# Performance work log

Measured on AMD Instinct MI355X. Metric: run time of the kernel, lower is better.

The kernel has to match this reference:

```python
import jax, jax.numpy as jnp
import numpy as np

N = 50000      # nodes
E = 800000     # edges (avg degree 16)
F_IN = 128
HID = 64
NCLS = 40
K = 2          # num_stacks
T = 2          # num_layers (shared weights)


def setup_inputs() -> dict:
    key = jax.random.key(0)
    ks = jax.random.split(key, 10)
    s = 0.05
    return {
        "x": jax.random.normal(ks[0], (N, F_IN), dtype=jnp.float32),
        "edge_index": jax.random.randint(ks[1], (2, E), 0, N),
        "w1_init": jax.random.normal(ks[2], (K, F_IN, HID), dtype=jnp.float32) * s,
        "w1": jax.random.normal(ks[3], (K, HID, HID), dtype=jnp.float32) * s,
        "v1": jax.random.normal(ks[4], (K, F_IN, HID), dtype=jnp.float32) * s,
        "b1": jax.random.normal(ks[5], (K, HID), dtype=jnp.float32) * s,
        "w2_init": jax.random.normal(ks[6], (K, HID, NCLS), dtype=jnp.float32) * s,
        "w2": jax.random.normal(ks[7], (K, NCLS, NCLS), dtype=jnp.float32) * s,
        "v2": jax.random.normal(ks[8], (K, HID, NCLS), dtype=jnp.float32) * s,
        "b2": jax.random.normal(ks[9], (K, NCLS), dtype=jnp.float32) * s,
    }


def _gcn_norm(src, dst, n):
    # PyG gcn_norm with add_self_loops=False: deg over destination, sym norm
    deg = jax.ops.segment_sum(jnp.ones_like(dst, dtype=jnp.float32), dst, num_segments=n)
    dinv = jnp.where(deg > 0, 1.0 / jnp.sqrt(deg), 0.0)
    return dinv[src] * dinv[dst]  # [E]


def _arma_conv(x, src, dst, norm, n, w_init, w, v, b, act):
    # x: [N, Fin]; w_init: [K, Fin, Fout]; w: [K, Fout, Fout]; v: [K, Fin, Fout]; b: [K, Fout]
    root = jnp.einsum('nf,kfg->kng', x, v)  # [K, N, Fout], dropout=0 -> identity
    out = None
    for t in range(T):
        if t == 0:
            h = jnp.einsum('nf,kfg->kng', x, w_init)
        else:
            h = jnp.einsum('knf,kfg->kng', out, w)
        # sparse neighbor aggregation: out[i] = sum_{(j->i)} norm_e * h[j]
        agg = jax.vmap(
            lambda hk: jax.ops.segment_sum(hk[src] * norm[:, None], dst, num_segments=n)
        )(h)  # [K, N, Fout]
        out = act(agg + root + b[:, None, :])
    return out.mean(axis=0)  # mean over stacks -> [N, Fout]


def reference(x, edge_index, w1_init, w1, v1, b1, w2_init, w2, v2, b2):
    src, dst = edge_index[0], edge_index[1]
    norm = _gcn_norm(src, dst, N)
    h = _arma_conv(x, src, dst, norm, N, w1_init, w1, v1, b1, jax.nn.relu)
    h = jax.nn.relu(h)  # wrapper ReLU; dropout is identity in eval
    o = _arma_conv(h, src, dst, norm, N, w2_init, w2, v2, b2, lambda z: z)
    return jax.nn.log_softmax(o, axis=1)
```

## Files before the change

### kernel.cpp

```cpp
#include <hip/hip_runtime.h>
#include <hip/hip_bf16.h>
#include <math.h>

#define N_NODES 50000
#define F_IN 128
#define HID 64
#define NCLS 40
#define K_STACKS 2
#define SCAN_TILE 1024
#define NBLK_CNT 256

typedef __attribute__((ext_vector_type(8))) short short8;
typedef __attribute__((ext_vector_type(4))) float floatx4;
typedef __attribute__((ext_vector_type(2))) float floatx2;

__device__ __forceinline__ unsigned int f32_to_bf16_bits(float f) {
    unsigned int u = __float_as_uint(f);
    return (u + 0x7fffu + ((u >> 16) & 1u)) >> 16;
}
__device__ __forceinline__ unsigned int pack_bf16x2(float a, float b) {
    return f32_to_bf16_bits(a) | (f32_to_bf16_bits(b) << 16);
}
__device__ __forceinline__ unsigned char f32_to_fp8(float v) {
    int pk = __builtin_amdgcn_cvt_pk_fp8_f32(v, v, 0, false);
    return (unsigned char)(pk & 0xff);
}


__global__ __launch_bounds__(256) void count_kernel(const int* __restrict__ dst,
                                                    int* __restrict__ counts,
                                                    int* __restrict__ tileSums, int E) {
    __shared__ int hist[256];
    __shared__ int ts[64];
    int blk = blockIdx.x, t = threadIdx.x;
    hist[t] = 0;
    if (t < 64) ts[t] = 0;
    __syncthreads();
    int chunk = (E + NBLK_CNT - 1) / NBLK_CNT;
    int s = blk * chunk, e = min(E, s + chunk);
    for (int i = s + t; i < e; i += 256) atomicAdd(&hist[dst[i] >> 8], 1);
    __syncthreads();
    counts[t * NBLK_CNT + blk] = hist[t];
    atomicAdd(&ts[t >> 2], hist[t]);
    __syncthreads();
    if (t < 64) atomicAdd(&tileSums[t], ts[t]);
}

__global__ __launch_bounds__(256) void scan_phase3_excl(const int* __restrict__ in,
                                                        const int* __restrict__ tileSums,
                                                        int* __restrict__ out, int n) {
    __shared__ int lds[256];
    __shared__ int tsum[64];
    int b = blockIdx.x, t = threadIdx.x;
    if (t < 64) tsum[t] = tileSums[t];
    int base = b * SCAN_TILE + t * 4;
    int e[4];
    int s = 0;
#pragma unroll
    for (int i = 0; i < 4; ++i) {
        e[i] = (base + i < n) ? in[base + i] : 0;
        s += e[i];
    }
    lds[t] = s;
    __syncthreads();
    int v = s;
    for (int off = 1; off < 256; off <<= 1) {
        int add = (t >= off) ? lds[t - off] : 0;
        __syncthreads();
        v += add;
        lds[t] = v;
        __syncthreads();
    }
    int toff = 0;
    for (int i = 0; i < b; ++i) toff += tsum[i];
    int run = (t == 0 ? 0 : lds[t - 1]) + toff;
#pragma unroll
    for (int i = 0; i < 4; ++i) {
        if (base + i < n) {
            out[base + i] = run;
            run += e[i];
        }
    }
}

__global__ __launch_bounds__(256) void bucket_scatter_kernel(const int* __restrict__ src,
                                                             const int* __restrict__ dst,
                                                             const int* __restrict__ scanned,
                                                             unsigned int* __restrict__ pairs,
                                                             int E) {
    __shared__ int cur[256];
    int blk = blockIdx.x, t = threadIdx.x;
    cur[t] = scanned[t * NBLK_CNT + blk];
    __syncthreads();
    int chunk = (E + NBLK_CNT - 1) / NBLK_CNT;
    int s0 = blk * chunk, e0 = min(E, s0 + chunk);
    for (int i = s0 + t; i < e0; i += 256) {
        int d = dst[i];
        int pos = atomicAdd(&cur[d >> 8], 1);
        pairs[pos] = (unsigned int)src[i] | ((unsigned int)(d & 255) << 16);
    }
}

__global__ __launch_bounds__(256) void csr_build_kernel(const unsigned int* __restrict__ pairs,
                                                        const int* __restrict__ scanned,
                                                        int* __restrict__ row_ptr,
                                                        float* __restrict__ dinv,
                                                        int* __restrict__ col, int N, int E) {
    __shared__ int degl[256], lds[256], curl[256], sb[2];
    int b = blockIdx.x, t = threadIdx.x;
    if (t == 0) {
        sb[0] = scanned[b * NBLK_CNT];
        sb[1] = (b + 1 < 256) ? scanned[(b + 1) * NBLK_CNT] : E;
    }
    degl[t] = 0;
    __syncthreads();
    int bstart = sb[0], bend = sb[1];
    for (int e = bstart + t; e < bend; e += 256) {
        atomicAdd(&degl[(pairs[e] >> 16) & 255], 1);
    }
    __syncthreads();
    int d = degl[t];
    lds[t] = d;
    __syncthreads();
    int v = d;
    for (int off = 1; off < 256; off <<= 1) {
        int add = (t >= off) ? lds[t - off] : 0;
        __syncthreads();
        v += add;
        lds[t] = v;
        __syncthreads();
    }
    int excl = v - d;
    int node = b * 256 + t;
    if (node <= N) row_ptr[node] = bstart + excl;
    if (node < N) dinv[node] = (d > 0) ? (1.0f / sqrtf((float)d)) : 0.0f;
    curl[t] = excl;
    __syncthreads();
    for (int e = bstart + t; e < bend; e += 256) {
        unsigned int p = pairs[e];
        int ln = (p >> 16) & 255;
        int pos = atomicAdd(&curl[ln], 1);
        col[bstart + pos] = (int)(p & 0xffffu);
    }
}

__device__ __forceinline__ void wt_one(const float* __restrict__ in,
                                       unsigned short* __restrict__ out, int li, int C, int F,
                                       int CP) {
    int k = li / (F * CP);
    int r = li - k * F * CP;
    int f = r / CP;
    int c = r - f * CP;
    out[li] = (c < C) ? (unsigned short)f32_to_bf16_bits(in[((size_t)k * C + c) * F + f]) : 0;
}

__global__ void wt_all_kernel(const float* v1, const float* w1i, const float* w1,
                              const float* v2, const float* w2i, const float* w2,
                              unsigned short* v1t, unsigned short* w1it, unsigned short* w1t,
                              unsigned short* v2t, unsigned short* w2it, unsigned short* w2t) {
    int i = blockIdx.x * blockDim.x + threadIdx.x;
    if (i < 16384) wt_one(v1, v1t, i, 128, 64, 128);
    else if (i < 32768) wt_one(w1i, w1it, i - 16384, 128, 64, 128);
    else if (i < 40960) wt_one(w1, w1t, i - 32768, 64, 64, 64);
    else if (i < 46080) wt_one(v2, v2t, i - 40960, 64, 40, 64);
    else if (i < 51200) wt_one(w2i, w2it, i - 46080, 64, 40, 64);
    else if (i < 56320) wt_one(w2, w2t, i - 51200, 40, 40, 64);
}

template <int CINP>
__device__ __forceinline__ void stage_A(const void* A, unsigned short* At, size_t abase,
                                        int n0, int t, int N, int CREAL, int a_bf16,
                                        int stride) {
    constexpr int CP8 = CINP / 8;
    constexpr int MS = CP8 - 1;
    constexpr int SH = (CP8 == 16) ? 4 : 3;
    for (int i = t; i < 64 * CP8; i += stride) {
        int n = i >> SH;
        int c = i & MS;
        uint4 w = make_uint4(0u, 0u, 0u, 0u);
        int gn = n0 + n;
        if (gn < N && c * 8 < CREAL) {
            if (a_bf16) {
                w = *(const uint4*)((const unsigned short*)A + abase + (size_t)gn * CREAL + c * 8);
            } else {
                const float* srcp = (const float*)A + abase + (size_t)gn * CREAL + c * 8;
                float4 f0 = *(const float4*)(srcp);
                float4 f1 = *(const float4*)(srcp + 4);
                w.x = pack_bf16x2(f0.x, f0.y);
                w.y = pack_bf16x2(f0.z, f0.w);
                w.z = pack_bf16x2(f1.x, f1.y);
                w.w = pack_bf16x2(f1.z, f1.w);
            }
        }
        *(uint4*)(At + n * CINP + ((c ^ (n & MS)) << 3)) = w;
    }
}

template <int CINP>
__device__ __forceinline__ void stage_B(const unsigned short* Bk, unsigned short* Bs, int t,
                                        int COUT, int stride) {
    constexpr int CP8 = CINP / 8;
    constexpr int MS = CP8 - 1;
    constexpr int SH = (CP8 == 16) ? 4 : 3;
    for (int i = t; i < COUT * CP8; i += stride) {
        int f = i >> SH;
        int c = i & MS;
        uint4 w = *(const uint4*)(Bk + f * CINP + c * 8);
        *(uint4*)(Bs + f * CINP + ((c ^ (f & MS)) << 3)) = w;
    }
}

__global__ __launch_bounds__(512) void gemm2k(
    const float* __restrict__ A, const unsigned short* __restrict__ Bt1,
    const unsigned short* __restrict__ Bt2, unsigned short* __restrict__ out1,
    unsigned char* __restrict__ out2, const float* __restrict__ scale, int N) {
    constexpr int CINP = 128;
    constexpr int MS = 15;
    __shared__ __align__(16) unsigned short At[64 * CINP];

    const int n0 = blockIdx.x * 64;
    const int t = threadIdx.x;
    stage_A<CINP>(A, At, (size_t)0, n0, t, N, CINP, 0, 512);
    __syncthreads();

    const int lane = t & 63;
    const int wv = t >> 6;
    const int kSel = wv >> 2;
    const int m0 = (wv & 3) * 16;
    const int quad = lane >> 4;
    const int li = lane & 15;
    const int am = (m0 + li) & MS;
    const unsigned short* B1k = Bt1 + (size_t)kSel * 64 * CINP;
    const unsigned short* B2k = Bt2 + (size_t)kSel * 64 * CINP;

    floatx4 acc1[4] = {{0.f, 0.f, 0.f, 0.f}, {0.f, 0.f, 0.f, 0.f},
                       {0.f, 0.f, 0.f, 0.f}, {0.f, 0.f, 0.f, 0.f}};
    floatx4 acc2[4] = {{0.f, 0.f, 0.f, 0.f}, {0.f, 0.f, 0.f, 0.f},
                       {0.f, 0.f, 0.f, 0.f}, {0.f, 0.f, 0.f, 0.f}};
#pragma unroll
    for (int kc = 0; kc < 4; ++kc) {
        int cc = kc * 4 + quad;
        short8 a = *(const short8*)(At + (m0 + li) * CINP + ((cc ^ am) << 3));
#pragma unroll
        for (int nt = 0; nt < 4; ++nt) {
            int f = nt * 16 + li;
            size_t bo = (size_t)f * CINP + cc * 8;
            short8 b1 = *(const short8*)(B1k + bo);
            short8 b2 = *(const short8*)(B2k + bo);
            acc1[nt] = __builtin_amdgcn_mfma_f32_16x16x32_bf16(a, b1, acc1[nt], 0, 0, 0);
            acc2[nt] = __builtin_amdgcn_mfma_f32_16x16x32_bf16(a, b2, acc2[nt], 0, 0, 0);
        }
    }

    float sc[4];
#pragma unroll
    for (int r = 0; r < 4; ++r) {
        int node = n0 + m0 + quad * 4 + r;
        sc[r] = (node < N) ? scale[node] : 1.f;
    }
#pragma unroll
    for (int nt = 0; nt < 4; ++nt) {
        int f = nt * 16 + li;
#pragma unroll
        for (int r = 0; r < 4; ++r) {
            int node = n0 + m0 + quad * 4 + r;
            if (node < N) {
                out1[((size_t)kSel * N + node) * 64 + f] =
                    (unsigned short)f32_to_bf16_bits(acc1[nt][r]);
                out2[(size_t)node * 128 + (size_t)kSel * 64 + f] =
                    f32_to_fp8(acc2[nt][r] * sc[r]);
            }
        }
    }
}

template <int F, int COUT, int FMODE>
__global__ __launch_bounds__(512) void agg_gemm_kernel(
    const unsigned char* __restrict__ h8, const int* __restrict__ row_ptr,
    const int* __restrict__ col, const float* __restrict__ dinv,
    const unsigned short* __restrict__ rootb, const float* __restrict__ bias,
    const unsigned short* __restrict__ Bt1, const unsigned short* __restrict__ Bt2,
    unsigned short* __restrict__ rootOut, unsigned char* __restrict__ tblOut, int N) {
    constexpr int NA = (FMODE == 1) ? 1 : 2;
    constexpr int NB = (FMODE == 1) ? 4 : 2;
    constexpr int BT = COUT * 64;
    constexpr int NT = (COUT + 15) / 16;
    constexpr int FH = F / 8;
    constexpr int ROWB = 2 * F;
    __shared__ __align__(16) unsigned short At[NA * 64 * 64];
    __shared__ __align__(16) unsigned short Bs[NB * BT];
    __shared__ int rp[65];
    __shared__ float dvl[64];

    const int n0 = blockIdx.x * 64;
    const int t = threadIdx.x;

    stage_B<64>(Bt1, Bs, t, COUT, 512);
    stage_B<64>(Bt1 + (size_t)COUT * 64, Bs + BT, t, COUT, 512);
    if constexpr (FMODE == 1) {
        stage_B<64>(Bt2, Bs + 2 * BT, t, COUT, 512);
        stage_B<64>(Bt2 + (size_t)COUT * 64, Bs + 3 * BT, t, COUT, 512);
    }
    if (t < 65) rp[t] = row_ptr[min(n0 + t, N)];
    if (t < 64) dvl[t] = (n0 + t < N) ? dinv[n0 + t] : 0.f;
    __syncthreads();

    const int lane = t & 63;
    const int wv = t >> 6;
    const int half = lane >> 5;
    const int l32 = lane & 31;
    const int sub = l32 >> 4;
    const int fq = l32 & 15;
    const int kk = fq >> 3;
    const int fqq = fq & 7;
    const int fqc = (fqq < FH) ? fqq : (FH - 1);
    const int foff = kk * F + fqc * 8;

#pragma unroll 1
    for (int p = 0; p < 4; ++p) {
        const int nl = wv * 8 + p * 2 + half;
        const int node = n0 + nl;
        const bool valid = node < N;
        const int e0 = rp[nl];
        const int deg = rp[nl + 1] - e0;
        const float dv = dvl[nl];
        float acc[8] = {};
        for (int w0 = 0; w0 < deg; w0 += 32) {
            int mye = w0 + l32;
            int c = (mye < deg) ? col[e0 + mye] : 0;
            int nch = min(deg - w0, 32);
            for (int base = 0; base < nch; base += 16) {
                uint2 v[8];
                float wj[8];
#pragma unroll
                for (int u = 0; u < 8; ++u) {
                    int j = base + u * 2 + sub;
                    int cj = __shfl(c, (half << 5) | (j & 31));
                    bool ok = (j < nch);
                    wj[u] = ok ? 1.f : 0.f;
                    int cs = ok ? cj : 0;
                    v[u] = *(const uint2*)(h8 + (size_t)cs * ROWB + foff);
                }
#pragma unroll
                for (int u = 0; u < 8; ++u) {
                    floatx2 f0 = __builtin_amdgcn_cvt_pk_f32_fp8(v[u].x, false);
                    floatx2 f1 = __builtin_amdgcn_cvt_pk_f32_fp8(v[u].x, true);
                    floatx2 f2 = __builtin_amdgcn_cvt_pk_f32_fp8(v[u].y, false);
                    floatx2 f3 = __builtin_amdgcn_cvt_pk_f32_fp8(v[u].y, true);
                    acc[0] += wj[u] * f0.x;
                    acc[1] += wj[u] * f0.y;
                    acc[2] += wj[u] * f1.x;
                    acc[3] += wj[u] * f1.y;
                    acc[4] += wj[u] * f2.x;
                    acc[5] += wj[u] * f2.y;
                    acc[6] += wj[u] * f3.x;
                    acc[7] += wj[u] * f3.y;
                }
            }
        }
#pragma unroll
        for (int i = 0; i < 8; ++i) acc[i] += __shfl_xor(acc[i], 16);

        size_t oc = ((size_t)kk * N + (valid ? node : 0)) * F + fqc * 8;
        uint4 rv = *(const uint4*)(rootb + oc);
        const float* bp = bias + kk * F + fqc * 8;
        float4 b0 = *(const float4*)(bp);
        float4 b1_ = *(const float4*)(bp + 4);
        const unsigned int ru[4] = {rv.x, rv.y, rv.z, rv.w};
        float res[8];
#pragma unroll
        for (int q = 0; q < 4; ++q) {
            float rlo = __uint_as_float(ru[q] << 16);
            float rhi = __uint_as_float(ru[q] & 0xffff0000u);
            float blo = (q < 2) ? ((q == 0) ? b0.x : b0.z) : ((q == 2) ? b1_.x : b1_.z);
            float bhi = (q < 2) ? ((q == 0) ? b0.y : b0.w) : ((q == 2) ? b1_.y : b1_.w);
            res[2 * q] = acc[2 * q] * dv + rlo + blo;
            res[2 * q + 1] = acc[2 * q + 1] * dv + rhi + bhi;
        }
        if constexpr (FMODE != 2) {
#pragma unroll
            for (int i = 0; i < 8; ++i) res[i] = fmaxf(res[i], 0.f);
        }
        if constexpr (FMODE == 1) {
            float mres[8];
#pragma unroll
            for (int i = 0; i < 8; ++i) mres[i] = 0.5f * (res[i] + __shfl_xor(res[i], 8));
            if (sub == 0 && kk == 0) {
                uint4 w;
                w.x = pack_bf16x2(mres[0], mres[1]);
                w.y = pack_bf16x2(mres[2], mres[3]);
                w.z = pack_bf16x2(mres[4], mres[5]);
                w.w = pack_bf16x2(mres[6], mres[7]);
                *(uint4*)(At + nl * 64 + ((fqq ^ (nl & 7)) << 3)) = w;
            }
        } else {
            if (sub == 0) {
                uint4 w = make_uint4(0u, 0u, 0u, 0u);
                if (fqq < FH) {
                    w.x = pack_bf16x2(res[0], res[1]);
                    w.y = pack_bf16x2(res[2], res[3]);
                    w.z = pack_bf16x2(res[4], res[5]);
                    w.w = pack_bf16x2(res[6], res[7]);
                }
                *(uint4*)(At + kk * 4096 + nl * 64 + ((fqq ^ (nl & 7)) << 3)) = w;
            }
        }
    }
    __syncthreads();

    const int quad = lane >> 4;
    const int li = lane & 15;
    const int kSel = wv >> 2;
    const int m0 = (wv & 3) * 16;
    const int am = (m0 + li) & 7;

    if constexpr (FMODE == 1) {
        floatx4 aR[NT] = {};
        floatx4 aT[NT] = {};
#pragma unroll
        for (int kc = 0; kc < 2; ++kc) {
            int cc = kc * 4 + quad;
            short8 a = *(const short8*)(At + (m0 + li) * 64 + ((cc ^ am) << 3));
#pragma unroll
            for (int nt = 0; nt < NT; ++nt) {
                int f = nt * 16 + li;
                int fc = (COUT & 15) ? ((f < COUT) ? f : (COUT - 1)) : f;
                int bo = fc * 64 + ((cc ^ (fc & 7)) << 3);
                short8 bR = *(const short8*)(Bs + kSel * BT + bo);
                short8 bT = *(const short8*)(Bs + (2 + kSel) * BT + bo);
                aR[nt] = __builtin_amdgcn_mfma_f32_16x16x32_bf16(a, bR, aR[nt], 0, 0, 0);
                aT[nt] = __builtin_amdgcn_mfma_f32_16x16x32_bf16(a, bT, aT[nt], 0, 0, 0);
            }
        }
#pragma unroll
        for (int nt = 0; nt < NT; ++nt) {
            int f = nt * 16 + li;
            if (f >= COUT) continue;
#pragma unroll
            for (int r = 0; r < 4; ++r) {
                int nl2 = m0 + quad * 4 + r;
                int node = n0 + nl2;
                if (node < N) {
                    rootOut[((size_t)kSel * N + node) * COUT + f] =
                        (unsigned short)f32_to_bf16_bits(aR[nt][r]);
                    tblOut[(size_t)node * 2 * COUT + (size_t)kSel * COUT + f] =
                        f32_to_fp8(aT[nt][r] * dvl[nl2]);
                }
            }
        }
    } else {
        floatx4 ac[NT] = {};
#pragma unroll
        for (int kc = 0; kc < 2; ++kc) {
            int cc = kc * 4 + quad;
            short8 a = *(const short8*)(At + kSel * 4096 + (m0 + li) * 64 + ((cc ^ am) << 3));
#pragma unroll
            for (int nt = 0; nt < NT; ++nt) {
                int f = nt * 16 + li;
                int fc = (COUT & 15) ? ((f < COUT) ? f : (COUT - 1)) : f;
                int bo = fc * 64 + ((cc ^ (fc & 7)) << 3);
                short8 b = *(const short8*)(Bs + kSel * BT + bo);
                ac[nt] = __builtin_amdgcn_mfma_f32_16x16x32_bf16(a, b, ac[nt], 0, 0, 0);
            }
        }
#pragma unroll
        for (int nt = 0; nt < NT; ++nt) {
            int f = nt * 16 + li;
            if (f >= COUT) continue;
#pragma unroll
            for (int r = 0; r < 4; ++r) {
                int nl2 = m0 + quad * 4 + r;
                int node = n0 + nl2;
                if (node < N)
                    tblOut[(size_t)node * 2 * COUT + (size_t)kSel * COUT + f] =
                        f32_to_fp8(ac[nt][r] * dvl[nl2]);
            }
        }
    }
}

template <int F>
__global__ __launch_bounds__(256) void agg_kernel(
    const unsigned char* __restrict__ h8, const int* __restrict__ row_ptr,
    const int* __restrict__ col, const float* __restrict__ dinv,
    const unsigned short* __restrict__ rootb, const float* __restrict__ bias,
    void* __restrict__ out, int N, int do_relu, int mode) {
    constexpr int FH = F / 8;
    constexpr int ROWB = 2 * F;
    int wid = (blockIdx.x * blockDim.x + threadIdx.x) >> 6;
    int lane = threadIdx.x & 63;
    int half = lane >> 5;
    int l32 = lane & 31;
    int node = wid * 2 + half;
    bool valid = node < N;
    int e0 = 0, deg = 0;
    float dv = 0.f;
    if (valid) {
        e0 = row_ptr[node];
        deg = row_ptr[node + 1] - e0;
        dv = dinv[node];
    }
    const int sub = l32 >> 4;
    const int fq = l32 & 15;
    const int kk = fq >> 3;
    const int fqq = fq & 7;
    const int fqc = (fqq < FH) ? fqq : (FH - 1);
    const int foff = kk * F + fqc * 8;

    float acc[8] = {};
    for (int w0 = 0; w0 < deg; w0 += 32) {
        int mye = w0 + l32;
        int c = (mye < deg) ? col[e0 + mye] : 0;
        int nch = min(deg - w0, 32);
        for (int base = 0; base < nch; base += 16) {
            uint2 v[8];
            float wj[8];
#pragma unroll
            for (int u = 0; u < 8; ++u) {
                int j = base + u * 2 + sub;
                int cj = __shfl(c, (half << 5) | (j & 31));
                bool ok = (j < nch);
                wj[u] = ok ? 1.f : 0.f;
                int cs = ok ? cj : 0;
                v[u] = *(const uint2*)(h8 + (size_t)cs * ROWB + foff);
            }
#pragma unroll
            for (int u = 0; u < 8; ++u) {
                floatx2 f0 = __builtin_amdgcn_cvt_pk_f32_fp8(v[u].x, false);
                floatx2 f1 = __builtin_amdgcn_cvt_pk_f32_fp8(v[u].x, true);
                floatx2 f2 = __builtin_amdgcn_cvt_pk_f32_fp8(v[u].y, false);
                floatx2 f3 = __builtin_amdgcn_cvt_pk_f32_fp8(v[u].y, true);
                acc[0] += wj[u] * f0.x;
                acc[1] += wj[u] * f0.y;
                acc[2] += wj[u] * f1.x;
                acc[3] += wj[u] * f1.y;
                acc[4] += wj[u] * f2.x;
                acc[5] += wj[u] * f2.y;
                acc[6] += wj[u] * f3.x;
                acc[7] += wj[u] * f3.y;
            }
        }
    }
#pragma unroll
    for (int i = 0; i < 8; ++i) acc[i] += __shfl_xor(acc[i], 16);

    size_t oc = ((size_t)kk * N + (valid ? node : 0)) * F + fqc * 8;
    uint4 rv = *(const uint4*)(rootb + oc);
    const float* bp = bias + kk * F + fqc * 8;
    float4 b0 = *(const float4*)(bp);
    float4 b1 = *(const float4*)(bp + 4);
    const unsigned int ru[4] = {rv.x, rv.y, rv.z, rv.w};
    float res[8];
#pragma unroll
    for (int q = 0; q < 4; ++q) {
        float rlo = __uint_as_float(ru[q] << 16);
        float rhi = __uint_as_float(ru[q] & 0xffff0000u);
        float blo = (q < 2) ? ((q == 0) ? b0.x : b0.z) : ((q == 2) ? b1.x : b1.z);
        float bhi = (q < 2) ? ((q == 0) ? b0.y : b0.w) : ((q == 2) ? b1.y : b1.w);
        res[2 * q] = acc[2 * q] * dv + rlo + blo;
        res[2 * q + 1] = acc[2 * q + 1] * dv + rhi + bhi;
    }
    if (do_relu) {
#pragma unroll
        for (int i = 0; i < 8; ++i) res[i] = fmaxf(res[i], 0.f);
    }
    if (mode == 0) {
        if (sub == 0 && fqq < FH && valid) {
            size_t o = ((size_t)kk * N + node) * F + fqq * 8;
            uint4 w;
            w.x = pack_bf16x2(res[0], res[1]);
            w.y = pack_bf16x2(res[2], res[3]);
            w.z = pack_bf16x2(res[4], res[5]);
            w.w = pack_bf16x2(res[6], res[7]);
            *(uint4*)((unsigned short*)out + o) = w;
        }
    } else {
        float mres[8];
#pragma unroll
        for (int i = 0; i < 8; ++i) mres[i] = 0.5f * (res[i] + __shfl_xor(res[i], 8));
        if (mode == 1) {
            if (sub == 0 && kk == 0 && fqq < FH && valid) {
                size_t o = (size_t)node * F + fqq * 8;
                *(float4*)((float*)out + o) = make_float4(mres[0], mres[1], mres[2], mres[3]);
                *(float4*)((float*)out + o + 4) = make_float4(mres[4], mres[5], mres[6], mres[7]);
            }
        } else {
            bool act = (fqq < FH);
            float lm = -INFINITY;
            if (act) {
#pragma unroll
                for (int i = 0; i < 8; ++i) lm = fmaxf(lm, mres[i]);
            }
#pragma unroll
            for (int m = 1; m < 8; m <<= 1) lm = fmaxf(lm, __shfl_xor(lm, m));
            float ls = 0.f;
            if (act) {
#pragma unroll
                for (int i = 0; i < 8; ++i) ls += expf(mres[i] - lm);
            }
#pragma unroll
            for (int m = 1; m < 8; m <<= 1) ls += __shfl_xor(ls, m);
            float lg = lm + logf(ls);
            if (sub == 0 && kk == 0 && act && valid) {
                size_t o = (size_t)node * F + fqq * 8;
                *(float4*)((float*)out + o) =
                    make_float4(mres[0] - lg, mres[1] - lg, mres[2] - lg, mres[3] - lg);
                *(float4*)((float*)out + o + 4) =
                    make_float4(mres[4] - lg, mres[5] - lg, mres[6] - lg, mres[7] - lg);
            }
        }
    }
}


static inline size_t align256(size_t x) { return (x + 255) & ~(size_t)255; }

extern "C" void kernel_launch(void* const* d_in, const int* in_sizes, int n_in,
                              void* d_out, int out_size, void* d_ws, size_t ws_size,
                              hipStream_t stream) {
    const float* x = (const float*)d_in[0];
    const int* ei = (const int*)d_in[1];
    const float* w1_init = (const float*)d_in[2];
    const float* w1 = (const float*)d_in[3];
    const float* v1 = (const float*)d_in[4];
    const float* b1 = (const float*)d_in[5];
    const float* w2_init = (const float*)d_in[6];
    const float* w2 = (const float*)d_in[7];
    const float* v2 = (const float*)d_in[8];
    const float* b2 = (const float*)d_in[9];

    const int N = in_sizes[0] / F_IN;
    const int E = in_sizes[1] / 2;
    const int* src = ei;
    const int* dst = ei + E;

    char* p = (char*)d_ws;
    auto take = [&](size_t bytes) {
        char* r = p;
        p += align256(bytes);
        return r;
    };
    float* dinv = (float*)take((size_t)N * 4);
    int* row_ptr = (int*)take((size_t)(N + 1) * 4);
    int* tileSums = (int*)take(256 * 4);
    int* counts = (int*)take((size_t)256 * NBLK_CNT * 4);
    int* scanned = (int*)take((size_t)256 * NBLK_CNT * 4);
    unsigned int* pairs = (unsigned int*)take((size_t)E * 4);
    int* col = (int*)take((size_t)E * 4);
    unsigned short* v1t = (unsigned short*)take((size_t)2 * 64 * 128 * 2);
    unsigned short* w1it = (unsigned short*)take((size_t)2 * 64 * 128 * 2);
    unsigned short* w1t = (unsigned short*)take((size_t)2 * 64 * 64 * 2);
    unsigned short* v2t = (unsigned short*)take((size_t)2 * 40 * 64 * 2);
    unsigned short* w2it = (unsigned short*)take((size_t)2 * 40 * 64 * 2);
    unsigned short* w2t = (unsigned short*)take((size_t)2 * 40 * 64 * 2);
    unsigned short* rootb = (unsigned short*)take((size_t)K_STACKS * N * HID * 2);
    unsigned short* root2 = (unsigned short*)take((size_t)K_STACKS * N * NCLS * 2);
    unsigned char* tblA = (unsigned char*)take((size_t)K_STACKS * N * HID);
    unsigned char* tblB = (unsigned char*)take((size_t)K_STACKS * N * HID);

    const int TB = 256;
    const int nCnt = 256 * NBLK_CNT;
    const int nScanBlocks = nCnt / SCAN_TILE;
    const int nBuckets = (N + 255) / 256;
    const int ntiles = (N + 63) / 64;

    hipMemsetAsync(tileSums, 0, 256, stream);
    count_kernel<<<NBLK_CNT, 256, 0, stream>>>(dst, counts, tileSums, E);
    scan_phase3_excl<<<nScanBlocks, 256, 0, stream>>>(counts, tileSums, scanned, nCnt);
    bucket_scatter_kernel<<<NBLK_CNT, 256, 0, stream>>>(src, dst, scanned, pairs, E);
    csr_build_kernel<<<nBuckets, 256, 0, stream>>>(pairs, scanned, row_ptr, dinv, col, N, E);

    wt_all_kernel<<<(56320 + TB - 1) / TB, TB, 0, stream>>>(v1, w1_init, w1, v2, w2_init, w2,
                                                            v1t, w1it, w1t, v2t, w2it, w2t);

    const int agg_blocks = ((N + 1) / 2 + 3) / 4;

    gemm2k<<<ntiles, 512, 0, stream>>>(x, v1t, w1it, rootb, tblA, dinv, N);
    agg_gemm_kernel<HID, HID, 0><<<ntiles, 512, 0, stream>>>(
        tblA, row_ptr, col, dinv, rootb, b1, w1t, nullptr, nullptr, tblB, N);

    agg_gemm_kernel<HID, NCLS, 1><<<ntiles, 512, 0, stream>>>(
        tblB, row_ptr, col, dinv, rootb, b1, v2t, w2it, root2, tblA, N);

    agg_gemm_kernel<NCLS, NCLS, 2><<<ntiles, 512, 0, stream>>>(
        tblA, row_ptr, col, dinv, root2, b2, w2t, nullptr, nullptr, tblB, N);

    agg_kernel<NCLS><<<agg_blocks, 256, 0, stream>>>(tblB, row_ptr, col, dinv, root2, b2,
                                                     (float*)d_out, N, 0, 2);
}
```

Measured before the change: 276.0 us.

## Drop LDS weight staging, process two rows per gather pass, fold memset into weight kernel

The fused aggregate+GEMM kernels no longer copy the B weight matrices into shared memory. MFMA operands are now read straight from global memory (expected to be cache-resident), which cuts LDS use, and the launch bounds request 4 blocks per CU. The neighbour gather now walks two destination rows at once, so more independent loads are in flight, and padding lanes are zeroed by select instead of multiply. The tileSums memset is folded into the weight-transpose kernel, which moves ahead of the CSR build, removing one launch. The risks are uncoalesced global B reads, more register pressure from the doubled accumulators, and wasted work when the two rows differ in degree.

```diff
diff --git a/kernel.cpp b/kernel.cpp
--- a/kernel.cpp
+++ b/kernel.cpp
@@ -157,8 +157,10 @@
 __global__ void wt_all_kernel(const float* v1, const float* w1i, const float* w1,
                               const float* v2, const float* w2i, const float* w2,
                               unsigned short* v1t, unsigned short* w1it, unsigned short* w1t,
-                              unsigned short* v2t, unsigned short* w2it, unsigned short* w2t) {
+                              unsigned short* v2t, unsigned short* w2it, unsigned short* w2t,
+                              int* tileSums) {
     int i = blockIdx.x * blockDim.x + threadIdx.x;
+    if (blockIdx.x == 0 && threadIdx.x < 64) tileSums[threadIdx.x] = 0;
     if (i < 16384) wt_one(v1, v1t, i, 128, 64, 128);
     else if (i < 32768) wt_one(w1i, w1it, i - 16384, 128, 64, 128);
     else if (i < 40960) wt_one(w1, w1t, i - 32768, 64, 64, 64);
@@ -196,20 +198,6 @@
     }
 }
 
-template <int CINP>
-__device__ __forceinline__ void stage_B(const unsigned short* Bk, unsigned short* Bs, int t,
-                                        int COUT, int stride) {
-    constexpr int CP8 = CINP / 8;
-    constexpr int MS = CP8 - 1;
-    constexpr int SH = (CP8 == 16) ? 4 : 3;
-    for (int i = t; i < COUT * CP8; i += stride) {
-        int f = i >> SH;
-        int c = i & MS;
-        uint4 w = *(const uint4*)(Bk + f * CINP + c * 8);
-        *(uint4*)(Bs + f * CINP + ((c ^ (f & MS)) << 3)) = w;
-    }
-}
-
 __global__ __launch_bounds__(512) void gemm2k(
     const float* __restrict__ A, const unsigned short* __restrict__ Bt1,
     const unsigned short* __restrict__ Bt2, unsigned short* __restrict__ out1,
@@ -275,34 +263,28 @@
 }
 
 template <int F, int COUT, int FMODE>
-__global__ __launch_bounds__(512) void agg_gemm_kernel(
+__global__ __launch_bounds__(512, 4) void agg_gemm_kernel(
     const unsigned char* __restrict__ h8, const int* __restrict__ row_ptr,
     const int* __restrict__ col, const float* __restrict__ dinv,
     const unsigned short* __restrict__ rootb, const float* __restrict__ bias,
     const unsigned short* __restrict__ Bt1, const unsigned short* __restrict__ Bt2,
     unsigned short* __restrict__ rootOut, unsigned char* __restrict__ tblOut, int N) {
     constexpr int NA = (FMODE == 1) ? 1 : 2;
-    constexpr int NB = (FMODE == 1) ? 4 : 2;
-    constexpr int BT = COUT * 64;
     constexpr int NT = (COUT + 15) / 16;
     constexpr int FH = F / 8;
     constexpr int ROWB = 2 * F;
     __shared__ __align__(16) unsigned short At[NA * 64 * 64];
-    __shared__ __align__(16) unsigned short Bs[NB * BT];
     __shared__ int rp[65];
     __shared__ float dvl[64];
 
     const int n0 = blockIdx.x * 64;
     const int t = threadIdx.x;
 
-    stage_B<64>(Bt1, Bs, t, COUT, 512);
-    stage_B<64>(Bt1 + (size_t)COUT * 64, Bs + BT, t, COUT, 512);
-    if constexpr (FMODE == 1) {
-        stage_B<64>(Bt2, Bs + 2 * BT, t, COUT, 512);
-        stage_B<64>(Bt2 + (size_t)COUT * 64, Bs + 3 * BT, t, COUT, 512);
-    }
     if (t < 65) rp[t] = row_ptr[min(n0 + t, N)];
-    if (t < 64) dvl[t] = (n0 + t < N) ? dinv[n0 + t] : 0.f;
+    if (t >= 128 && t < 192) {
+        int i = t - 128;
+        dvl[i] = (n0 + i < N) ? dinv[n0 + i] : 0.f;
+    }
     __syncthreads();
 
     const int lane = t & 63;
@@ -316,51 +298,12 @@
     const int fqc = (fqq < FH) ? fqq : (FH - 1);
     const int foff = kk * F + fqc * 8;
 
-#pragma unroll 1
-    for (int p = 0; p < 4; ++p) {
-        const int nl = wv * 8 + p * 2 + half;
+    auto finish_row = [&](int nl, float* acc) {
         const int node = n0 + nl;
         const bool valid = node < N;
-        const int e0 = rp[nl];
-        const int deg = rp[nl + 1] - e0;
         const float dv = dvl[nl];
-        float acc[8] = {};
-        for (int w0 = 0; w0 < deg; w0 += 32) {
-            int mye = w0 + l32;
-            int c = (mye < deg) ? col[e0 + mye] : 0;
-            int nch = min(deg - w0, 32);
-            for (int base = 0; base < nch; base += 16) {
-                uint2 v[8];
-                float wj[8];
-#pragma unroll
-                for (int u = 0; u < 8; ++u) {
-                    int j = base + u * 2 + sub;
-                    int cj = __shfl(c, (half << 5) | (j & 31));
-                    bool ok = (j < nch);
-                    wj[u] = ok ? 1.f : 0.f;
-                    int cs = ok ? cj : 0;
-                    v[u] = *(const uint2*)(h8 + (size_t)cs * ROWB + foff);
-                }
-#pragma unroll
-                for (int u = 0; u < 8; ++u) {
-                    floatx2 f0 = __builtin_amdgcn_cvt_pk_f32_fp8(v[u].x, false);
-                    floatx2 f1 = __builtin_amdgcn_cvt_pk_f32_fp8(v[u].x, true);
-                    floatx2 f2 = __builtin_amdgcn_cvt_pk_f32_fp8(v[u].y, false);
-                    floatx2 f3 = __builtin_amdgcn_cvt_pk_f32_fp8(v[u].y, true);
-                    acc[0] += wj[u] * f0.x;
-                    acc[1] += wj[u] * f0.y;
-                    acc[2] += wj[u] * f1.x;
-                    acc[3] += wj[u] * f1.y;
-                    acc[4] += wj[u] * f2.x;
-                    acc[5] += wj[u] * f2.y;
-                    acc[6] += wj[u] * f3.x;
-                    acc[7] += wj[u] * f3.y;
-                }
-            }
-        }
 #pragma unroll
         for (int i = 0; i < 8; ++i) acc[i] += __shfl_xor(acc[i], 16);
-
         size_t oc = ((size_t)kk * N + (valid ? node : 0)) * F + fqc * 8;
         uint4 rv = *(const uint4*)(rootb + oc);
         const float* bp = bias + kk * F + fqc * 8;
@@ -405,6 +348,68 @@
                 *(uint4*)(At + kk * 4096 + nl * 64 + ((fqq ^ (nl & 7)) << 3)) = w;
             }
         }
+    };
+
+#pragma unroll 1
+    for (int p = 0; p < 2; ++p) {
+        const int nlA = wv * 8 + p * 4 + half;
+        const int nlB = nlA + 2;
+        const int e0A = rp[nlA];
+        const int degA = rp[nlA + 1] - e0A;
+        const int e0B = rp[nlB];
+        const int degB = rp[nlB + 1] - e0B;
+        const int degM = max(degA, degB);
+        float accA[8] = {};
+        float accB[8] = {};
+        for (int w0 = 0; w0 < degM; w0 += 32) {
+            int mye = w0 + l32;
+            int cA = (mye < degA) ? col[e0A + mye] : 0;
+            int cB = (mye < degB) ? col[e0B + mye] : 0;
+            int nchA = degA - w0;
+            int nchB = degB - w0;
+            if (nchA > 32) nchA = 32;
+            if (nchB > 32) nchB = 32;
+            int nchM = min(degM - w0, 32);
+            for (int base = 0; base < nchM; base += 16) {
+                uint2 vA[8], vB[8];
+#pragma unroll
+                for (int u = 0; u < 8; ++u) {
+                    int j = base + u * 2 + sub;
+                    int li32 = (half << 5) | (j & 31);
+                    int cjA = __shfl(cA, li32);
+                    int cjB = __shfl(cB, li32);
+                    bool okA = (j < nchA);
+                    bool okB = (j < nchB);
+                    uint2 tA = *(const uint2*)(h8 + (size_t)(okA ? cjA : 0) * ROWB + foff);
+                    uint2 tB = *(const uint2*)(h8 + (size_t)(okB ? cjB : 0) * ROWB + foff);
+                    vA[u].x = okA ? tA.x : 0u;
+                    vA[u].y = okA ? tA.y : 0u;
+                    vB[u].x = okB ? tB.x : 0u;
+                    vB[u].y = okB ? tB.y : 0u;
+                }
+#pragma unroll
+                for (int u = 0; u < 8; ++u) {
+                    floatx2 a0 = __builtin_amdgcn_cvt_pk_f32_fp8(vA[u].x, false);
+                    floatx2 a1 = __builtin_amdgcn_cvt_pk_f32_fp8(vA[u].x, true);
+                    floatx2 a2 = __builtin_amdgcn_cvt_pk_f32_fp8(vA[u].y, false);
+                    floatx2 a3 = __builtin_amdgcn_cvt_pk_f32_fp8(vA[u].y, true);
+                    accA[0] += a0.x; accA[1] += a0.y;
+                    accA[2] += a1.x; accA[3] += a1.y;
+                    accA[4] += a2.x; accA[5] += a2.y;
+                    accA[6] += a3.x; accA[7] += a3.y;
+                    floatx2 c0 = __builtin_amdgcn_cvt_pk_f32_fp8(vB[u].x, false);
+                    floatx2 c1 = __builtin_amdgcn_cvt_pk_f32_fp8(vB[u].x, true);
+                    floatx2 c2 = __builtin_amdgcn_cvt_pk_f32_fp8(vB[u].y, false);
+                    floatx2 c3 = __builtin_amdgcn_cvt_pk_f32_fp8(vB[u].y, true);
+                    accB[0] += c0.x; accB[1] += c0.y;
+                    accB[2] += c1.x; accB[3] += c1.y;
+                    accB[4] += c2.x; accB[5] += c2.y;
+                    accB[6] += c3.x; accB[7] += c3.y;
+                }
+            }
+        }
+        finish_row(nlA, accA);
+        finish_row(nlB, accB);
     }
     __syncthreads();
 
@@ -413,8 +418,10 @@
     const int kSel = wv >> 2;
     const int m0 = (wv & 3) * 16;
     const int am = (m0 + li) & 7;
+    const unsigned short* B1k = Bt1 + (size_t)kSel * COUT * 64;
 
     if constexpr (FMODE == 1) {
+        const unsigned short* B2k = Bt2 + (size_t)kSel * COUT * 64;
         floatx4 aR[NT] = {};
         floatx4 aT[NT] = {};
 #pragma unroll
@@ -424,10 +431,10 @@
 #pragma unroll
             for (int nt = 0; nt < NT; ++nt) {
                 int f = nt * 16 + li;
-                int fc = (COUT & 15) ? ((f < COUT) ? f : (COUT - 1)) : f;
-                int bo = fc * 64 + ((cc ^ (fc & 7)) << 3);
-                short8 bR = *(const short8*)(Bs + kSel * BT + bo);
-                short8 bT = *(const short8*)(Bs + (2 + kSel) * BT + bo);
+                int fc = (f < COUT) ? f : (COUT - 1);
+                size_t bo = (size_t)fc * 64 + cc * 8;
+                short8 bR = *(const short8*)(B1k + bo);
+                short8 bT = *(const short8*)(B2k + bo);
                 aR[nt] = __builtin_amdgcn_mfma_f32_16x16x32_bf16(a, bR, aR[nt], 0, 0, 0);
                 aT[nt] = __builtin_amdgcn_mfma_f32_16x16x32_bf16(a, bT, aT[nt], 0, 0, 0);
             }
@@ -457,9 +464,9 @@
 #pragma unroll
             for (int nt = 0; nt < NT; ++nt) {
                 int f = nt * 16 + li;
-                int fc = (COUT & 15) ? ((f < COUT) ? f : (COUT - 1)) : f;
-                int bo = fc * 64 + ((cc ^ (fc & 7)) << 3);
-                short8 b = *(const short8*)(Bs + kSel * BT + bo);
+                int fc = (f < COUT) ? f : (COUT - 1);
+                size_t bo = (size_t)fc * 64 + cc * 8;
+                short8 b = *(const short8*)(B1k + bo);
                 ac[nt] = __builtin_amdgcn_mfma_f32_16x16x32_bf16(a, b, ac[nt], 0, 0, 0);
             }
         }
@@ -664,15 +671,14 @@
     const int nBuckets = (N + 255) / 256;
     const int ntiles = (N + 63) / 64;
 
-    hipMemsetAsync(tileSums, 0, 256, stream);
+    wt_all_kernel<<<(56320 + TB - 1) / TB, TB, 0, stream>>>(v1, w1_init, w1, v2, w2_init, w2,
+                                                            v1t, w1it, w1t, v2t, w2it, w2t,
+                                                            tileSums);
     count_kernel<<<NBLK_CNT, 256, 0, stream>>>(dst, counts, tileSums, E);
     scan_phase3_excl<<<nScanBlocks, 256, 0, stream>>>(counts, tileSums, scanned, nCnt);
     bucket_scatter_kernel<<<NBLK_CNT, 256, 0, stream>>>(src, dst, scanned, pairs, E);
     csr_build_kernel<<<nBuckets, 256, 0, stream>>>(pairs, scanned, row_ptr, dinv, col, N, E);
 
-    wt_all_kernel<<<(56320 + TB - 1) / TB, TB, 0, stream>>>(v1, w1_init, w1, v2, w2_init, w2,
-                                                            v1t, w1it, w1t, v2t, w2it, w2t);
-
     const int agg_blocks = ((N + 1) / 2 + 3) / 4;
 
     gemm2k<<<ntiles, 512, 0, stream>>>(x, v1t, w1it, rootb, tblA, dinv, N);
```

After: 290.8 us. 5.4% more time.

## Split fp8 feature tables per stack and read weights from global

Applied to the files above, without the earlier changes.

The fp8 neighbor tables change from node-interleaved [N][2*F] to stack-major [K][N][F]. The first layer-1 aggregation+GEMM is split into two per-stack kernels so each gather touches a smaller 3.2MB table that fits better in cache. Weight tiles are no longer staged in LDS; MFMA operands are loaded straight from global/L2, which reduces shared memory use. The tileSums memset is folded into the weight-transpose kernel, removing one launch. The risks are an extra kernel launch, extra reads of col/row_ptr and rootb, and unswizzled global B loads.

```diff
diff --git a/kernel.cpp b/kernel.cpp
--- a/kernel.cpp
+++ b/kernel.cpp
@@ -157,8 +157,10 @@
 __global__ void wt_all_kernel(const float* v1, const float* w1i, const float* w1,
                               const float* v2, const float* w2i, const float* w2,
                               unsigned short* v1t, unsigned short* w1it, unsigned short* w1t,
-                              unsigned short* v2t, unsigned short* w2it, unsigned short* w2t) {
+                              unsigned short* v2t, unsigned short* w2it, unsigned short* w2t,
+                              int* tileSums) {
     int i = blockIdx.x * blockDim.x + threadIdx.x;
+    if (blockIdx.x == 0 && threadIdx.x < 64) tileSums[threadIdx.x] = 0;
     if (i < 16384) wt_one(v1, v1t, i, 128, 64, 128);
     else if (i < 32768) wt_one(w1i, w1it, i - 16384, 128, 64, 128);
     else if (i < 40960) wt_one(w1, w1t, i - 32768, 64, 64, 64);
@@ -196,20 +198,6 @@
     }
 }
 
-template <int CINP>
-__device__ __forceinline__ void stage_B(const unsigned short* Bk, unsigned short* Bs, int t,
-                                        int COUT, int stride) {
-    constexpr int CP8 = CINP / 8;
-    constexpr int MS = CP8 - 1;
-    constexpr int SH = (CP8 == 16) ? 4 : 3;
-    for (int i = t; i < COUT * CP8; i += stride) {
-        int f = i >> SH;
-        int c = i & MS;
-        uint4 w = *(const uint4*)(Bk + f * CINP + c * 8);
-        *(uint4*)(Bs + f * CINP + ((c ^ (f & MS)) << 3)) = w;
-    }
-}
-
 __global__ __launch_bounds__(512) void gemm2k(
     const float* __restrict__ A, const unsigned short* __restrict__ Bt1,
     const unsigned short* __restrict__ Bt2, unsigned short* __restrict__ out1,
@@ -267,9 +255,137 @@
             if (node < N) {
                 out1[((size_t)kSel * N + node) * 64 + f] =
                     (unsigned short)f32_to_bf16_bits(acc1[nt][r]);
-                out2[(size_t)node * 128 + (size_t)kSel * 64 + f] =
+                out2[((size_t)kSel * N + node) * 64 + f] =
                     f32_to_fp8(acc2[nt][r] * sc[r]);
             }
+        }
+    }
+}
+
+template <int KONLY>
+__global__ __launch_bounds__(512) void agg_gemm_k1(
+    const unsigned char* __restrict__ h8, const int* __restrict__ row_ptr,
+    const int* __restrict__ col, const float* __restrict__ dinv,
+    const unsigned short* __restrict__ rootb, const float* __restrict__ bias,
+    const unsigned short* __restrict__ Bt1, unsigned char* __restrict__ tblOut, int N) {
+    __shared__ __align__(16) unsigned short At[64 * 64];
+    __shared__ int rp[65];
+    __shared__ float dvl[64];
+
+    const int n0 = blockIdx.x * 64;
+    const int t = threadIdx.x;
+    if (t < 65) rp[t] = row_ptr[min(n0 + t, N)];
+    if (t >= 128 && t < 192) {
+        int i = t - 128;
+        dvl[i] = (n0 + i < N) ? dinv[n0 + i] : 0.f;
+    }
+    __syncthreads();
+
+    const int lane = t & 63;
+    const int wv = t >> 6;
+    const int half = lane >> 5;
+    const int l32 = lane & 31;
+    const int sub2 = l32 >> 3;
+    const int fqq = l32 & 7;
+    const unsigned char* h8k = h8 + (size_t)KONLY * N * 64;
+
+#pragma unroll 1
+    for (int p = 0; p < 4; ++p) {
+        const int nl = wv * 8 + p * 2 + half;
+        const int node = n0 + nl;
+        const bool valid = node < N;
+        const int e0 = rp[nl];
+        const int deg = rp[nl + 1] - e0;
+        const float dv = dvl[nl];
+        float acc[8] = {};
+        for (int w0 = 0; w0 < deg; w0 += 32) {
+            int mye = w0 + l32;
+            int c = (mye < deg) ? col[e0 + mye] : 0;
+            int nch = min(deg - w0, 32);
+            uint2 v[8];
+#pragma unroll
+            for (int u = 0; u < 8; ++u) {
+                int j = u * 4 + sub2;
+                int cj = __shfl(c, (half << 5) | j);
+                bool ok = (j < nch);
+                uint2 tv = *(const uint2*)(h8k + (size_t)(ok ? cj : 0) * 64 + fqq * 8);
+                v[u].x = ok ? tv.x : 0u;
+                v[u].y = ok ? tv.y : 0u;
+            }
+#pragma unroll
+            for (int u = 0; u < 8; ++u) {
+                floatx2 f0 = __builtin_amdgcn_cvt_pk_f32_fp8(v[u].x, false);
+                floatx2 f1 = __builtin_amdgcn_cvt_pk_f32_fp8(v[u].x, true);
+                floatx2 f2 = __builtin_amdgcn_cvt_pk_f32_fp8(v[u].y, false);
+                floatx2 f3 = __builtin_amdgcn_cvt_pk_f32_fp8(v[u].y, true);
+                acc[0] += f0.x; acc[1] += f0.y;
+                acc[2] += f1.x; acc[3] += f1.y;
+                acc[4] += f2.x; acc[5] += f2.y;
+                acc[6] += f3.x; acc[7] += f3.y;
+            }
+        }
+#pragma unroll
+        for (int i = 0; i < 8; ++i) {
+            acc[i] += __shfl_xor(acc[i], 8);
+            acc[i] += __shfl_xor(acc[i], 16);
+        }
+
+        size_t oc = ((size_t)KONLY * N + (valid ? node : 0)) * 64 + fqq * 8;
+        uint4 rv = *(const uint4*)(rootb + oc);
+        const float* bp = bias + KONLY * 64 + fqq * 8;
+        float4 b0 = *(const float4*)(bp);
+        float4 b1_ = *(const float4*)(bp + 4);
+        const unsigned int ru[4] = {rv.x, rv.y, rv.z, rv.w};
+        float res[8];
+#pragma unroll
+        for (int q = 0; q < 4; ++q) {
+            float rlo = __uint_as_float(ru[q] << 16);
+            float rhi = __uint_as_float(ru[q] & 0xffff0000u);
+            float blo = (q < 2) ? ((q == 0) ? b0.x : b0.z) : ((q == 2) ? b1_.x : b1_.z);
+            float bhi = (q < 2) ? ((q == 0) ? b0.y : b0.w) : ((q == 2) ? b1_.y : b1_.w);
+            res[2 * q] = fmaxf(acc[2 * q] * dv + rlo + blo, 0.f);
+            res[2 * q + 1] = fmaxf(acc[2 * q + 1] * dv + rhi + bhi, 0.f);
+        }
+        if (sub2 == 0) {
+            uint4 w;
+            w.x = pack_bf16x2(res[0], res[1]);
+            w.y = pack_bf16x2(res[2], res[3]);
+            w.z = pack_bf16x2(res[4], res[5]);
+            w.w = pack_bf16x2(res[6], res[7]);
+            *(uint4*)(At + nl * 64 + ((fqq ^ (nl & 7)) << 3)) = w;
+        }
+    }
+    __syncthreads();
+
+    const int quad = lane >> 4;
+    const int li = lane & 15;
+    const int m0 = (wv & 3) * 16;
+    const int ntBase = (wv >> 2) * 2;
+    const int am = (m0 + li) & 7;
+    const unsigned short* B1k = Bt1 + (size_t)KONLY * 64 * 64;
+
+    floatx4 ac[2] = {};
+#pragma unroll
+    for (int kc = 0; kc < 2; ++kc) {
+        int cc = kc * 4 + quad;
+        short8 a = *(const short8*)(At + (m0 + li) * 64 + ((cc ^ am) << 3));
+#pragma unroll
+        for (int nti = 0; nti < 2; ++nti) {
+            int f = (ntBase + nti) * 16 + li;
+            size_t bo = (size_t)f * 64 + cc * 8;
+            short8 b = *(const short8*)(B1k + bo);
+            ac[nti] = __builtin_amdgcn_mfma_f32_16x16x32_bf16(a, b, ac[nti], 0, 0, 0);
+        }
+    }
+#pragma unroll
+    for (int nti = 0; nti < 2; ++nti) {
+        int f = (ntBase + nti) * 16 + li;
+#pragma unroll
+        for (int r = 0; r < 4; ++r) {
+            int nl2 = m0 + quad * 4 + r;
+            int node = n0 + nl2;
+            if (node < N)
+                tblOut[((size_t)KONLY * N + node) * 64 + f] = f32_to_fp8(ac[nti][r] * dvl[nl2]);
         }
     }
 }
@@ -282,27 +398,19 @@
     const unsigned short* __restrict__ Bt1, const unsigned short* __restrict__ Bt2,
     unsigned short* __restrict__ rootOut, unsigned char* __restrict__ tblOut, int N) {
     constexpr int NA = (FMODE == 1) ? 1 : 2;
-    constexpr int NB = (FMODE == 1) ? 4 : 2;
-    constexpr int BT = COUT * 64;
     constexpr int NT = (COUT + 15) / 16;
     constexpr int FH = F / 8;
-    constexpr int ROWB = 2 * F;
     __shared__ __align__(16) unsigned short At[NA * 64 * 64];
-    __shared__ __align__(16) unsigned short Bs[NB * BT];
     __shared__ int rp[65];
     __shared__ float dvl[64];
 
     const int n0 = blockIdx.x * 64;
     const int t = threadIdx.x;
-
-    stage_B<64>(Bt1, Bs, t, COUT, 512);
-    stage_B<64>(Bt1 + (size_t)COUT * 64, Bs + BT, t, COUT, 512);
-    if constexpr (FMODE == 1) {
-        stage_B<64>(Bt2, Bs + 2 * BT, t, COUT, 512);
-        stage_B<64>(Bt2 + (size_t)COUT * 64, Bs + 3 * BT, t, COUT, 512);
-    }
     if (t < 65) rp[t] = row_ptr[min(n0 + t, N)];
-    if (t < 64) dvl[t] = (n0 + t < N) ? dinv[n0 + t] : 0.f;
+    if (t >= 128 && t < 192) {
+        int i = t - 128;
+        dvl[i] = (n0 + i < N) ? dinv[n0 + i] : 0.f;
+    }
     __syncthreads();
 
     const int lane = t & 63;
@@ -314,7 +422,8 @@
     const int kk = fq >> 3;
     const int fqq = fq & 7;
     const int fqc = (fqq < FH) ? fqq : (FH - 1);
-    const int foff = kk * F + fqc * 8;
+    const unsigned char* h8k = h8 + (size_t)kk * N * F;
+    const int foff = fqc * 8;
 
 #pragma unroll 1
     for (int p = 0; p < 4; ++p) {
@@ -339,7 +448,7 @@
                     bool ok = (j < nch);
                     wj[u] = ok ? 1.f : 0.f;
                     int cs = ok ? cj : 0;
-                    v[u] = *(const uint2*)(h8 + (size_t)cs * ROWB + foff);
+                    v[u] = *(const uint2*)(h8k + (size_t)cs * F + foff);
                 }
 #pragma unroll
                 for (int u = 0; u < 8; ++u) {
@@ -413,8 +522,10 @@
     const int kSel = wv >> 2;
     const int m0 = (wv & 3) * 16;
     const int am = (m0 + li) & 7;
+    const unsigned short* B1k = Bt1 + (size_t)kSel * COUT * 64;
 
     if constexpr (FMODE == 1) {
+        const unsigned short* B2k = Bt2 + (size_t)kSel * COUT * 64;
         floatx4 aR[NT] = {};
         floatx4 aT[NT] = {};
 #pragma unroll
@@ -424,10 +535,10 @@
 #pragma unroll
             for (int nt = 0; nt < NT; ++nt) {
                 int f = nt * 16 + li;
-                int fc = (COUT & 15) ? ((f < COUT) ? f : (COUT - 1)) : f;
-                int bo = fc * 64 + ((cc ^ (fc & 7)) << 3);
-                short8 bR = *(const short8*)(Bs + kSel * BT + bo);
-                short8 bT = *(const short8*)(Bs + (2 + kSel) * BT + bo);
+                int fc = (f < COUT) ? f : (COUT - 1);
+                size_t bo = (size_t)fc * 64 + cc * 8;
+                short8 bR = *(const short8*)(B1k + bo);
+                short8 bT = *(const short8*)(B2k + bo);
                 aR[nt] = __builtin_amdgcn_mfma_f32_16x16x32_bf16(a, bR, aR[nt], 0, 0, 0);
                 aT[nt] = __builtin_amdgcn_mfma_f32_16x16x32_bf16(a, bT, aT[nt], 0, 0, 0);
             }
@@ -443,7 +554,7 @@
                 if (node < N) {
                     rootOut[((size_t)kSel * N + node) * COUT + f] =
                         (unsigned short)f32_to_bf16_bits(aR[nt][r]);
-                    tblOut[(size_t)node * 2 * COUT + (size_t)kSel * COUT + f] =
+                    tblOut[((size_t)kSel * N + node) * COUT + f] =
                         f32_to_fp8(aT[nt][r] * dvl[nl2]);
                 }
             }
@@ -457,9 +568,9 @@
 #pragma unroll
             for (int nt = 0; nt < NT; ++nt) {
                 int f = nt * 16 + li;
-                int fc = (COUT & 15) ? ((f < COUT) ? f : (COUT - 1)) : f;
-                int bo = fc * 64 + ((cc ^ (fc & 7)) << 3);
-                short8 b = *(const short8*)(Bs + kSel * BT + bo);
+                int fc = (f < COUT) ? f : (COUT - 1);
+                size_t bo = (size_t)fc * 64 + cc * 8;
+                short8 b = *(const short8*)(B1k + bo);
                 ac[nt] = __builtin_amdgcn_mfma_f32_16x16x32_bf16(a, b, ac[nt], 0, 0, 0);
             }
         }
@@ -472,7 +583,7 @@
                 int nl2 = m0 + quad * 4 + r;
                 int node = n0 + nl2;
                 if (node < N)
-                    tblOut[(size_t)node * 2 * COUT + (size_t)kSel * COUT + f] =
+                    tblOut[((size_t)kSel * N + node) * COUT + f] =
                         f32_to_fp8(ac[nt][r] * dvl[nl2]);
             }
         }
@@ -484,9 +595,8 @@
     const unsigned char* __restrict__ h8, const int* __restrict__ row_ptr,
     const int* __restrict__ col, const float* __restrict__ dinv,
     const unsigned short* __restrict__ rootb, const float* __restrict__ bias,
-    void* __restrict__ out, int N, int do_relu, int mode) {
+    void* __restrict__ out, int N) {
     constexpr int FH = F / 8;
-    constexpr int ROWB = 2 * F;
     int wid = (blockIdx.x * blockDim.x + threadIdx.x) >> 6;
     int lane = threadIdx.x & 63;
     int half = lane >> 5;
@@ -505,7 +615,8 @@
     const int kk = fq >> 3;
     const int fqq = fq & 7;
     const int fqc = (fqq < FH) ? fqq : (FH - 1);
-    const int foff = kk * F + fqc * 8;
+    const unsigned char* h8k = h8 + (size_t)kk * N * F;
+    const int foff = fqc * 8;
 
     float acc[8] = {};
     for (int w0 = 0; w0 < deg; w0 += 32) {
@@ -522,7 +633,7 @@
                 bool ok = (j < nch);
                 wj[u] = ok ? 1.f : 0.f;
                 int cs = ok ? cj : 0;
-                v[u] = *(const uint2*)(h8 + (size_t)cs * ROWB + foff);
+                v[u] = *(const uint2*)(h8k + (size_t)cs * F + foff);
             }
 #pragma unroll
             for (int u = 0; u < 8; ++u) {
@@ -560,55 +671,31 @@
         res[2 * q] = acc[2 * q] * dv + rlo + blo;
         res[2 * q + 1] = acc[2 * q + 1] * dv + rhi + bhi;
     }
-    if (do_relu) {
-#pragma unroll
-        for (int i = 0; i < 8; ++i) res[i] = fmaxf(res[i], 0.f);
-    }
-    if (mode == 0) {
-        if (sub == 0 && fqq < FH && valid) {
-            size_t o = ((size_t)kk * N + node) * F + fqq * 8;
-            uint4 w;
-            w.x = pack_bf16x2(res[0], res[1]);
-            w.y = pack_bf16x2(res[2], res[3]);
-            w.z = pack_bf16x2(res[4], res[5]);
-            w.w = pack_bf16x2(res[6], res[7]);
-            *(uint4*)((unsigned short*)out + o) = w;
-        }
-    } else {
-        float mres[8];
-#pragma unroll
-        for (int i = 0; i < 8; ++i) mres[i] = 0.5f * (res[i] + __shfl_xor(res[i], 8));
-        if (mode == 1) {
-            if (sub == 0 && kk == 0 && fqq < FH && valid) {
-                size_t o = (size_t)node * F + fqq * 8;
-                *(float4*)((float*)out + o) = make_float4(mres[0], mres[1], mres[2], mres[3]);
-                *(float4*)((float*)out + o + 4) = make_float4(mres[4], mres[5], mres[6], mres[7]);
-            }
-        } else {
-            bool act = (fqq < FH);
-            float lm = -INFINITY;
-            if (act) {
-#pragma unroll
-                for (int i = 0; i < 8; ++i) lm = fmaxf(lm, mres[i]);
-            }
-#pragma unroll
-            for (int m = 1; m < 8; m <<= 1) lm = fmaxf(lm, __shfl_xor(lm, m));
-            float ls = 0.f;
-            if (act) {
-#pragma unroll
-                for (int i = 0; i < 8; ++i) ls += expf(mres[i] - lm);
-            }
-#pragma unroll
-            for (int m = 1; m < 8; m <<= 1) ls += __shfl_xor(ls, m);
-            float lg = lm + logf(ls);
-            if (sub == 0 && kk == 0 && act && valid) {
-                size_t o = (size_t)node * F + fqq * 8;
-                *(float4*)((float*)out + o) =
-                    make_float4(mres[0] - lg, mres[1] - lg, mres[2] - lg, mres[3] - lg);
-                *(float4*)((float*)out + o + 4) =
-                    make_float4(mres[4] - lg, mres[5] - lg, mres[6] - lg, mres[7] - lg);
-            }
-        }
+    float mres[8];
+#pragma unroll
+    for (int i = 0; i < 8; ++i) mres[i] = 0.5f * (res[i] + __shfl_xor(res[i], 8));
+    bool act = (fqq < FH);
+    float lm = -INFINITY;
+    if (act) {
+#pragma unroll
+        for (int i = 0; i < 8; ++i) lm = fmaxf(lm, mres[i]);
+    }
+#pragma unroll
+    for (int m = 1; m < 8; m <<= 1) lm = fmaxf(lm, __shfl_xor(lm, m));
+    float ls = 0.f;
+    if (act) {
+#pragma unroll
+        for (int i = 0; i < 8; ++i) ls += expf(mres[i] - lm);
+    }
+#pragma unroll
+    for (int m = 1; m < 8; m <<= 1) ls += __shfl_xor(ls, m);
+    float lg = lm + logf(ls);
+    if (sub == 0 && kk == 0 && act && valid) {
+        size_t o = (size_t)node * F + fqq * 8;
+        *(float4*)((float*)out + o) =
+            make_float4(mres[0] - lg, mres[1] - lg, mres[2] - lg, mres[3] - lg);
+        *(float4*)((float*)out + o + 4) =
+            make_float4(mres[4] - lg, mres[5] - lg, mres[6] - lg, mres[7] - lg);
     }
 }
 
@@ -664,20 +751,19 @@
     const int nBuckets = (N + 255) / 256;
     const int ntiles = (N + 63) / 64;
 
-    hipMemsetAsync(tileSums, 0, 256, stream);
+    wt_all_kernel<<<(56320 + TB - 1) / TB, TB, 0, stream>>>(v1, w1_init, w1, v2, w2_init, w2,
+                                                            v1t, w1it, w1t, v2t, w2it, w2t,
+                                                            tileSums);
     count_kernel<<<NBLK_CNT, 256, 0, stream>>>(dst, counts, tileSums, E);
     scan_phase3_excl<<<nScanBlocks, 256, 0, stream>>>(counts, tileSums, scanned, nCnt);
     bucket_scatter_kernel<<<NBLK_CNT, 256, 0, stream>>>(src, dst, scanned, pairs, E);
     csr_build_kernel<<<nBuckets, 256, 0, stream>>>(pairs, scanned, row_ptr, dinv, col, N, E);
 
-    wt_all_kernel<<<(56320 + TB - 1) / TB, TB, 0, stream>>>(v1, w1_init, w1, v2, w2_init, w2,
-                                                            v1t, w1it, w1t, v2t, w2it, w2t);
-
     const int agg_blocks = ((N + 1) / 2 + 3) / 4;
 
     gemm2k<<<ntiles, 512, 0, stream>>>(x, v1t, w1it, rootb, tblA, dinv, N);
-    agg_gemm_kernel<HID, HID, 0><<<ntiles, 512, 0, stream>>>(
-        tblA, row_ptr, col, dinv, rootb, b1, w1t, nullptr, nullptr, tblB, N);
+    agg_gemm_k1<0><<<ntiles, 512, 0, stream>>>(tblA, row_ptr, col, dinv, rootb, b1, w1t, tblB, N);
+    agg_gemm_k1<1><<<ntiles, 512, 0, stream>>>(tblA, row_ptr, col, dinv, rootb, b1, w1t, tblB, N);
 
     agg_gemm_kernel<HID, NCLS, 1><<<ntiles, 512, 0, stream>>>(
         tblB, row_ptr, col, dinv, rootb, b1, v2t, w2it, root2, tblA, N);
@@ -686,5 +772,5 @@
         tblA, row_ptr, col, dinv, root2, b2, w2t, nullptr, nullptr, tblB, N);
 
     agg_kernel<NCLS><<<agg_blocks, 256, 0, stream>>>(tblB, row_ptr, col, dinv, root2, b2,
-                                                     (float*)d_out, N, 0, 2);
-}
+                                                     (float*)d_out, N);
+}
```

After: 306.6 us. 1.11x slower.
